# Kernel tuning notes

Measured on AMD Instinct MI355X. Metric: run time of the kernel, lower is better.

The kernel has to match this reference:

```python
import jax, jax.numpy as jnp
import numpy as np

PH, PW = 7, 7  # pooled_height, pooled_width
B, H, W, C, R = 4, 64, 64, 256, 128


def setup_inputs() -> dict:
    key = jax.random.key(0)
    k1, k2, k3 = jax.random.split(key, 3)
    feature_map = jax.random.normal(k1, (B, H, W, C), dtype=jnp.float32)
    # ROIs: (y_min, x_min, y_max, x_max) relative coords; sized so every
    # region has >= PH rows / PW cols (avoids empty-bin -inf edge case).
    start = jax.random.uniform(k2, (B, R, 2), minval=0.0, maxval=0.4)
    extent = jax.random.uniform(k3, (B, R, 2), minval=0.3, maxval=0.55)
    rois = jnp.concatenate([start, start + extent], axis=-1).astype(jnp.float32)
    return {"feature_map": feature_map, "rois": rois}


def _pool_image(fm, rois_img):
    # fm: (H, W, C); rois_img: (R, 4)
    h, w, _ = fm.shape
    # tf.cast(float->int32) truncates; coords are non-negative so == floor
    h0 = jnp.floor(h * rois_img[:, 0]).astype(jnp.int32)
    w0 = jnp.floor(w * rois_img[:, 1]).astype(jnp.int32)
    h1 = jnp.floor(h * rois_img[:, 2]).astype(jnp.int32)
    w1 = jnp.floor(w * rois_img[:, 3]).astype(jnp.int32)
    rh, rw = h1 - h0, w1 - w0
    hstep = jnp.maximum(rh // PH, 1)  # guard: assumes region >= pooled grid
    wstep = jnp.maximum(rw // PW, 1)

    # Map each absolute row/col to its pooled bin (or PH/PW = "outside").
    rel_h = jnp.arange(h)[None, :] - h0[:, None]            # (R, H)
    bin_h = jnp.clip(rel_h // hstep[:, None], 0, PH - 1)     # last bin extends to region end
    row_id = jnp.where((rel_h >= 0) & (rel_h < rh[:, None]), bin_h, PH)
    rel_w = jnp.arange(w)[None, :] - w0[:, None]            # (R, W)
    bin_w = jnp.clip(rel_w // wstep[:, None], 0, PW - 1)
    col_id = jnp.where((rel_w >= 0) & (rel_w < rw[:, None]), bin_w, PW)

    # Stage 1: segment-max over rows -> (R, PH, W, C)
    seg_rows = jax.vmap(
        lambda ids: jax.ops.segment_max(fm, ids, num_segments=PH + 1)
    )(row_id)[:, :PH]

    # Stage 2: segment-max over cols -> (R, PH, PW, C)
    def col_pool(t, ids):  # t: (PH, W, C)
        tt = jnp.swapaxes(t, 0, 1)  # (W, PH, C)
        s = jax.ops.segment_max(tt, ids, num_segments=PW + 1)[:PW]
        return jnp.swapaxes(s, 0, 1)  # (PH, PW, C)

    return jax.vmap(col_pool)(seg_rows, col_id)


def reference(feature_map, rois):
    # (B, R, PH, PW, C)
    return jax.vmap(_pool_image)(feature_map, rois)
```

## Files before the change

kernel.cpp:

```cpp
#include <hip/hip_runtime.h>
#include <math.h>

#define PH 7
#define PW 7
#define BB 4
#define HH 64
#define WW 64
#define CC 256
#define RR 128
#define CH4 (CC / 4)
#define BINS_PER_IMG (RR * PH * PW)
#define NBINS (BB * BINS_PER_IMG)
#define NBLK 2048
#define BLK_HALF 256
#define WPI 2048

typedef float f4 __attribute__((ext_vector_type(4)));

__device__ __forceinline__ f4 max4(f4 a, f4 b) {
    f4 r;
    r.x = fmaxf(a.x, b.x); r.y = fmaxf(a.y, b.y);
    r.z = fmaxf(a.z, b.z); r.w = fmaxf(a.w, b.w);
    return r;
}
__device__ __forceinline__ int rfl(int x) { return __builtin_amdgcn_readfirstlane(x); }

__global__ __launch_bounds__(256, 8) void ROIPoolingLayer_62079457296467_kernel(
    const float* __restrict__ fm, const float* __restrict__ rois,
    float* __restrict__ out)
{
    const int lane = threadIdx.x & 63;
    const int wave = rfl((int)threadIdx.x >> 6);

    const int bid   = blockIdx.x;
    const int xcd   = bid & 7;
    const int b     = xcd >> 1;
    const int blkin = (xcd & 1) * BLK_HALF + (bid >> 3);
    const int wv    = blkin * 4 + wave;

    const f4* __restrict__ fmb  = (const f4*)fm + (size_t)b * (HH * WW) * CH4 + lane;
    const f4* __restrict__ roib = (const f4*)rois + (size_t)b * RR;
    f4* __restrict__ outb = (f4*)out + (size_t)b * BINS_PER_IMG * CH4 + lane;

#pragma unroll
    for (int t = 0; t < 4; ++t) {
        const int local = wv + t * WPI;
        if (local < BINS_PER_IMG) {
            const int r   = local / (PH * PW);
            const int bin = local - r * (PH * PW);
            const int ph  = bin / PW;
            const int pw  = bin - ph * PW;

            const f4 roi = roib[r];
            const int h0 = rfl((int)floorf((float)HH * roi.x));
            const int w0 = rfl((int)floorf((float)WW * roi.y));
            const int h1 = rfl((int)floorf((float)HH * roi.z));
            const int w1 = rfl((int)floorf((float)WW * roi.w));
            const int rh = h1 - h0, rw = w1 - w0;
            const int hstep = max(rh / PH, 1), wstep = max(rw / PW, 1);

            int hs = h0 + ph * hstep;
            int he = (ph == PH - 1) ? (h0 + rh) : (hs + hstep);
            he = min(he, h0 + rh);  he = min(he, HH);
            int ws = w0 + pw * wstep;
            int we = (pw == PW - 1) ? (w0 + rw) : (ws + wstep);
            we = min(we, w0 + rw);  we = min(we, WW);

            const int wbin = we - ws;
            const int npix = (he - hs) * wbin;
            f4 acc = (f4){-INFINITY, -INFINITY, -INFINITY, -INFINITY};

            if (npix > 0) {
                const int sbase = rfl(hs * WW + ws);
                const unsigned m = (65536u + (unsigned)wbin - 1) / (unsigned)wbin;
                for (int p = 0; p < npix; p += 8) {
                    f4 v[8];
#pragma unroll
                    for (int k = 0; k < 8; ++k) {
                        const int pk  = min(p + k, npix - 1);
                        const int q   = (int)(((unsigned)pk * m) >> 16);
                        const int off = rfl(sbase + q * WW + (pk - q * wbin));
                        v[k] = fmb[(size_t)off * CH4];
                    }
#pragma unroll
                    for (int k = 0; k < 4; ++k) v[k] = max4(v[k], v[k + 4]);
                    acc = max4(acc, max4(max4(v[0], v[1]), max4(v[2], v[3])));
                }
            }

            __builtin_nontemporal_store(acc, outb + (size_t)local * CH4);
        }
    }
}

extern "C" void kernel_launch(void* const* d_in, const int* in_sizes, int n_in,
                              void* d_out, int out_size, void* d_ws, size_t ws_size,
                              hipStream_t stream) {
    const float* fm   = (const float*)d_in[0];
    const float* rois = (const float*)d_in[1];
    float* out        = (float*)d_out;
    ROIPoolingLayer_62079457296467_kernel<<<NBLK, 256, 0, stream>>>(fm, rois, out);
}
```

Baseline: 91.97 us.

## Precompute bin descriptors in a separate kernel and pool two bins per wave

```diff
diff --git a/kernel.cpp b/kernel.cpp
--- a/kernel.cpp
+++ b/kernel.cpp
@@ -11,11 +11,13 @@
 #define CH4 (CC / 4)
 #define BINS_PER_IMG (RR * PH * PW)
 #define NBINS (BB * BINS_PER_IMG)
-#define NBLK 2048
-#define BLK_HALF 256
-#define WPI 2048
+#define DESC_BYTES ((size_t)NBINS * 16)
+#define MAIN_BLK 3136
+#define WAVES_PER_IMG 3136
+#define BLK_HALF 392
 
 typedef float f4 __attribute__((ext_vector_type(4)));
+typedef int   i4 __attribute__((ext_vector_type(4)));
 
 __device__ __forceinline__ f4 max4(f4 a, f4 b) {
     f4 r;
@@ -25,72 +27,121 @@
 }
 __device__ __forceinline__ int rfl(int x) { return __builtin_amdgcn_readfirstlane(x); }
 
-__global__ __launch_bounds__(256, 8) void ROIPoolingLayer_62079457296467_kernel(
-    const float* __restrict__ fm, const float* __restrict__ rois,
+__global__ __launch_bounds__(256) void desc_kernel(
+    const float* __restrict__ rois, i4* __restrict__ desc)
+{
+    const int gbin = blockIdx.x * 256 + threadIdx.x;
+    const int br  = gbin / (PH * PW);
+    const int bin = gbin - br * (PH * PW);
+    const int b   = br >> 7;
+    const int ph  = bin / PW;
+    const int pw  = bin - ph * PW;
+
+    const f4 roi = ((const f4*)rois)[br];
+    const int h0 = (int)floorf((float)HH * roi.x);
+    const int w0 = (int)floorf((float)WW * roi.y);
+    const int h1 = (int)floorf((float)HH * roi.z);
+    const int w1 = (int)floorf((float)WW * roi.w);
+    const int rh = h1 - h0, rw = w1 - w0;
+    const int hstep = max(rh / PH, 1), wstep = max(rw / PW, 1);
+
+    int hs = h0 + ph * hstep;
+    int he = (ph == PH - 1) ? (h0 + rh) : (hs + hstep);
+    he = min(he, h0 + rh);  he = min(he, HH);
+    int ws = w0 + pw * wstep;
+    int we = (pw == PW - 1) ? (w0 + rw) : (ws + wstep);
+    we = min(we, w0 + rw);  we = min(we, WW);
+
+    const int hbin = he - hs, wbin = we - ws;
+    const int npix = (hbin > 0 && wbin > 0) ? hbin * wbin : 0;
+    const int wb   = max(wbin, 1);
+    i4 d;
+    d.x = (b * HH + hs) * WW + ws;
+    d.y = npix;
+    d.z = wb;
+    d.w = (int)((65536u + (unsigned)wb - 1) / (unsigned)wb);
+    desc[gbin] = d;
+}
+
+__global__ __launch_bounds__(256, 4) void ROIPoolingLayer_62079457296467_kernel(
+    const float* __restrict__ fm, const i4* __restrict__ desc,
     float* __restrict__ out)
 {
     const int lane = threadIdx.x & 63;
     const int wave = rfl((int)threadIdx.x >> 6);
 
-    const int bid   = blockIdx.x;
-    const int xcd   = bid & 7;
-    const int b     = xcd >> 1;
-    const int blkin = (xcd & 1) * BLK_HALF + (bid >> 3);
-    const int wv    = blkin * 4 + wave;
+    const int bid  = blockIdx.x;
+    const int xcd  = bid & 7;
+    const int b    = xcd >> 1;
+    const int inb  = (xcd & 1) * BLK_HALF + (bid >> 3);
+    const int gw   = b * WAVES_PER_IMG + inb * 4 + wave;
+    const int g0   = 2 * gw;
+    const int g1   = g0 + 1;
 
-    const f4* __restrict__ fmb  = (const f4*)fm + (size_t)b * (HH * WW) * CH4 + lane;
-    const f4* __restrict__ roib = (const f4*)rois + (size_t)b * RR;
-    f4* __restrict__ outb = (f4*)out + (size_t)b * BINS_PER_IMG * CH4 + lane;
+    const i4 d0 = desc[g0];
+    const i4 d1 = desc[g1];
+    const int n0 = rfl(d0.y), n1 = rfl(d1.y);
 
+    const f4* __restrict__ fm4 = (const f4*)fm + lane;
+    f4 acc0 = (f4){-INFINITY, -INFINITY, -INFINITY, -INFINITY};
+    f4 acc1 = acc0;
+
+    if (n0 > 0 && n1 > 0) {
+        const int s0 = rfl(d0.x), w0b = rfl(d0.z);
+        const int s1 = rfl(d1.x), w1b = rfl(d1.z);
+        const unsigned m0 = (unsigned)rfl(d0.w), m1 = (unsigned)rfl(d1.w);
+        const int pmax = max(n0, n1);
+        for (int p = 0; p < pmax; p += 8) {
+            f4 v0[8], v1[8];
 #pragma unroll
-    for (int t = 0; t < 4; ++t) {
-        const int local = wv + t * WPI;
-        if (local < BINS_PER_IMG) {
-            const int r   = local / (PH * PW);
-            const int bin = local - r * (PH * PW);
-            const int ph  = bin / PW;
-            const int pw  = bin - ph * PW;
-
-            const f4 roi = roib[r];
-            const int h0 = rfl((int)floorf((float)HH * roi.x));
-            const int w0 = rfl((int)floorf((float)WW * roi.y));
-            const int h1 = rfl((int)floorf((float)HH * roi.z));
-            const int w1 = rfl((int)floorf((float)WW * roi.w));
-            const int rh = h1 - h0, rw = w1 - w0;
-            const int hstep = max(rh / PH, 1), wstep = max(rw / PW, 1);
-
-            int hs = h0 + ph * hstep;
-            int he = (ph == PH - 1) ? (h0 + rh) : (hs + hstep);
-            he = min(he, h0 + rh);  he = min(he, HH);
-            int ws = w0 + pw * wstep;
-            int we = (pw == PW - 1) ? (w0 + rw) : (ws + wstep);
-            we = min(we, w0 + rw);  we = min(we, WW);
-
-            const int wbin = we - ws;
-            const int npix = (he - hs) * wbin;
-            f4 acc = (f4){-INFINITY, -INFINITY, -INFINITY, -INFINITY};
-
-            if (npix > 0) {
-                const int sbase = rfl(hs * WW + ws);
-                const unsigned m = (65536u + (unsigned)wbin - 1) / (unsigned)wbin;
-                for (int p = 0; p < npix; p += 8) {
-                    f4 v[8];
+            for (int k = 0; k < 8; ++k) {
+                const int pk = min(p + k, n0 - 1);
+                const int q  = (int)(((unsigned)pk * m0) >> 16);
+                const int off = rfl(s0 + q * WW + (pk - q * w0b));
+                v0[k] = fm4[(size_t)off * CH4];
+            }
 #pragma unroll
-                    for (int k = 0; k < 8; ++k) {
-                        const int pk  = min(p + k, npix - 1);
-                        const int q   = (int)(((unsigned)pk * m) >> 16);
-                        const int off = rfl(sbase + q * WW + (pk - q * wbin));
-                        v[k] = fmb[(size_t)off * CH4];
-                    }
+            for (int k = 0; k < 8; ++k) {
+                const int pk = min(p + k, n1 - 1);
+                const int q  = (int)(((unsigned)pk * m1) >> 16);
+                const int off = rfl(s1 + q * WW + (pk - q * w1b));
+                v1[k] = fm4[(size_t)off * CH4];
+            }
 #pragma unroll
-                    for (int k = 0; k < 4; ++k) v[k] = max4(v[k], v[k + 4]);
-                    acc = max4(acc, max4(max4(v[0], v[1]), max4(v[2], v[3])));
+            for (int k = 0; k < 4; ++k) v0[k] = max4(v0[k], v0[k + 4]);
+            acc0 = max4(acc0, max4(max4(v0[0], v0[1]), max4(v0[2], v0[3])));
+#pragma unroll
+            for (int k = 0; k < 4; ++k) v1[k] = max4(v1[k], v1[k + 4]);
+            acc1 = max4(acc1, max4(max4(v1[0], v1[1]), max4(v1[2], v1[3])));
+        }
+    } else {
+        for (int t = 0; t < 2; ++t) {
+            const i4 d = t ? d1 : d0;
+            const int n = rfl(d.y);
+            if (n <= 0) continue;
+            const int sb = rfl(d.x), wb = rfl(d.z);
+            const unsigned m = (unsigned)rfl(d.w);
+            f4 a = (f4){-INFINITY, -INFINITY, -INFINITY, -INFINITY};
+            for (int p = 0; p < n; p += 8) {
+                f4 v[8];
+#pragma unroll
+                for (int k = 0; k < 8; ++k) {
+                    const int pk = min(p + k, n - 1);
+                    const int q  = (int)(((unsigned)pk * m) >> 16);
+                    const int off = rfl(sb + q * WW + (pk - q * wb));
+                    v[k] = fm4[(size_t)off * CH4];
                 }
+#pragma unroll
+                for (int k = 0; k < 4; ++k) v[k] = max4(v[k], v[k + 4]);
+                a = max4(a, max4(max4(v[0], v[1]), max4(v[2], v[3])));
             }
-
-            __builtin_nontemporal_store(acc, outb + (size_t)local * CH4);
+            if (t) acc1 = a; else acc0 = a;
         }
     }
+
+    f4* o = (f4*)out + (size_t)g0 * CH4 + lane;
+    __builtin_nontemporal_store(acc0, o);
+    __builtin_nontemporal_store(acc1, o + CH4);
 }
 
 extern "C" void kernel_launch(void* const* d_in, const int* in_sizes, int n_in,
@@ -99,5 +150,7 @@
     const float* fm   = (const float*)d_in[0];
     const float* rois = (const float*)d_in[1];
     float* out        = (float*)d_out;
-    ROIPoolingLayer_62079457296467_kernel<<<NBLK, 256, 0, stream>>>(fm, rois, out);
+    i4* desc          = (i4*)d_ws;
+    desc_kernel<<<NBINS / 256, 256, 0, stream>>>(rois, desc);
+    ROIPoolingLayer_62079457296467_kernel<<<MAIN_BLK, 256, 0, stream>>>(fm, desc, out);
 }
```

Result: slower. 97.40 us (+5.9%).
